# Kernel tuning notes

Hardware: AMD Instinct MI355X
Metric: run time of the kernel (lower is better)

The kernel has to match this reference:

```python
import jax, jax.numpy as jnp
import numpy as np

N_DIM = 512
HIDDEN = 512


def setup_inputs() -> dict:
    key = jax.random.key(0)
    ks = jax.random.split(key, 9)
    s = 0.02
    x = jax.random.normal(ks[0], (4, 4096, N_DIM), dtype=jnp.float32)
    Wq = jax.random.normal(ks[1], (N_DIM, HIDDEN), dtype=jnp.float32) * s
    bq = jnp.zeros((HIDDEN,), dtype=jnp.float32)
    Wk = jax.random.normal(ks[2], (N_DIM, HIDDEN), dtype=jnp.float32) * s
    bk = jnp.zeros((HIDDEN,), dtype=jnp.float32)
    Wv = jax.random.normal(ks[3], (N_DIM, HIDDEN), dtype=jnp.float32) * s
    bv = jnp.zeros((HIDDEN,), dtype=jnp.float32)
    Wo = jax.random.normal(ks[4], (HIDDEN, N_DIM), dtype=jnp.float32) * s
    bo = jnp.zeros((N_DIM,), dtype=jnp.float32)
    return {"x": x, "Wq": Wq, "bq": bq, "Wk": Wk, "bk": bk,
            "Wv": Wv, "bv": bv, "Wo": Wo, "bo": bo}


def reference(x, Wq, bq, Wk, bk, Wv, bv, Wo, bo):
    # x: [B, S, n_dim]
    q = jnp.einsum('bsd,dh->bsh', x, Wq) + bq  # [B,S,H]
    k = jnp.einsum('bsd,dh->bsh', x, Wk) + bk
    v = jnp.einsum('bsd,dh->bsh', x, Wv) + bv
    # NOTE: original module uses UNSCALED scores (no 1/sqrt(d))
    scores = jnp.einsum('bqh,bkh->bqk', q, k)  # [B,S,S]
    attn = jax.nn.softmax(scores, axis=-1)
    y = jnp.einsum('bqk,bkh->bqh', attn, v)
    return jnp.einsum('bsh,hd->bsd', y, Wo) + bo
```

## Files before the change

kernel.cpp:

```cpp
#include <hip/hip_runtime.h>
#include <hip/hip_bf16.h>

typedef _Float16 h8 __attribute__((ext_vector_type(8)));
typedef __bf16   b8 __attribute__((ext_vector_type(8)));
typedef float    f4 __attribute__((ext_vector_type(4)));

#define B_    4
#define S_    4096
#define D_    512
#define ROWS_ (B_ * S_)
#define NQKV_ 1536
#define BR    64
#define BC    32
#define KP    520
#define PP    40
#define NIT   (S_ / BC)
#define KTILE (BC * KP)
#define MSH   (30.0f * 1.4426950408889634f)
#define L2E   1.4426950408889634f

__device__ __forceinline__ void gl_lds16(const void* src, void* dst) {
    __builtin_amdgcn_global_load_lds(
        (const __attribute__((address_space(1))) unsigned int*)src,
        (__attribute__((address_space(3))) unsigned int*)dst, 16, 0, 0);
}

__global__ __launch_bounds__(256) void convert_all(
    const float* __restrict__ x,
    const float* __restrict__ Wq, const float* __restrict__ Wk, const float* __restrict__ Wv,
    const float* __restrict__ bq, const float* __restrict__ bk, const float* __restrict__ bv,
    const float* __restrict__ Wo,
    _Float16* __restrict__ xh, _Float16* __restrict__ wqkvT, _Float16* __restrict__ woT,
    float* __restrict__ bqkv)
{
    long i0 = (long)blockIdx.x * blockDim.x + threadIdx.x;
    long stride = (long)gridDim.x * blockDim.x;
    const long NX  = (long)ROWS_ * D_;
    const long NW  = (long)D_ * NQKV_;
    const long NWO = (long)D_ * D_;

    for (long i = i0; i < NX; i += stride) xh[i] = (_Float16)x[i];

    for (long i = i0; i < NW; i += stride) {
        long n = i >> 9, k = i & 511;
        long which = n >> 9, nn = n & 511;
        const float* W = (which == 0) ? Wq : (which == 1) ? Wk : Wv;
        wqkvT[i] = (_Float16)W[k * 512 + nn];
    }
    for (long i = i0; i < NWO; i += stride) {
        long n = i >> 9, k = i & 511;
        woT[i] = (_Float16)Wo[k * 512 + n];
    }
    for (long i = i0; i < NQKV_; i += stride) {
        long which = i >> 9, nn = i & 511;
        const float* bb = (which == 0) ? bq : (which == 1) ? bk : bv;
        bqkv[i] = bb[nn];
    }
}

#define GP 40
template <bool OUT_F16>
__global__ __launch_bounds__(256) void gemm_bt(
    const _Float16* __restrict__ A, const _Float16* __restrict__ BT,
    const float* __restrict__ bias, void* __restrict__ Cout,
    int M, int N, int K)
{
    __shared__ _Float16 As[128 * GP];
    __shared__ _Float16 Bs[128 * GP];

    int tid = threadIdx.x;
    int w = tid >> 6, lane = tid & 63, quad = lane >> 4, l16 = lane & 15;
    long row0 = (long)blockIdx.x * 128, col0 = (long)blockIdx.y * 128;
    int wr = (w >> 1) * 64, wc = (w & 1) * 64;

    f4 acc[4][4];
    for (int i = 0; i < 4; i++)
        for (int j = 0; j < 4; j++) acc[i][j] = (f4){0.f, 0.f, 0.f, 0.f};

    int sr = tid >> 1, sc = (tid & 1) * 16;
    for (int k0 = 0; k0 < K; k0 += 32) {
        __syncthreads();
        {
            const h8* ga = (const h8*)(A  + (row0 + sr) * K + k0 + sc);
            const h8* gb = (const h8*)(BT + (col0 + sr) * K + k0 + sc);
            *(h8*)(As + sr * GP + sc)     = ga[0];
            *(h8*)(As + sr * GP + sc + 8) = ga[1];
            *(h8*)(Bs + sr * GP + sc)     = gb[0];
            *(h8*)(Bs + sr * GP + sc + 8) = gb[1];
        }
        __syncthreads();
        h8 af[4], bf[4];
        for (int i = 0; i < 4; i++) af[i] = *(const h8*)(As + (wr + i * 16 + l16) * GP + quad * 8);
        for (int j = 0; j < 4; j++) bf[j] = *(const h8*)(Bs + (wc + j * 16 + l16) * GP + quad * 8);
        for (int i = 0; i < 4; i++)
            for (int j = 0; j < 4; j++)
                acc[i][j] = __builtin_amdgcn_mfma_f32_16x16x32_f16(af[i], bf[j], acc[i][j], 0, 0, 0);
    }
    for (int i = 0; i < 4; i++)
        for (int j = 0; j < 4; j++)
            for (int r = 0; r < 4; r++) {
                long row = row0 + wr + i * 16 + quad * 4 + r;
                long col = col0 + wc + j * 16 + l16;
                float v = acc[i][j][r] + bias[col];
                if (OUT_F16) ((_Float16*)Cout)[row * N + col] = (_Float16)v;
                else         ((float*)Cout)[row * N + col]    = v;
            }
}

__global__ __launch_bounds__(256) void pack_v(const _Float16* __restrict__ qkv,
                                              __bf16* __restrict__ vP)
{
    __shared__ _Float16 T[32 * 520];
    int kt = blockIdx.x, b = blockIdx.y;
    int t = threadIdx.x;

    const _Float16* src = qkv + ((long)b * S_ + kt * 32 + (t >> 3)) * NQKV_ + 1024;
#pragma unroll
    for (int i = 0; i < 8; i++) {
        int c = (t & 7) + i * 8;
        *(h8*)(T + (t >> 3) * 520 + c * 8) = *(const h8*)(src + c * 8);
    }
    __syncthreads();

    __bf16* dst = vP + (((long)b * 128 + kt) * 32) * 512;
#pragma unroll
    for (int i = 0; i < 8; i++) {
        int c = t + i * 256;
        int dt = c >> 6, q = (c >> 4) & 3, l = c & 15;
        b8 out;
#pragma unroll
        for (int k3 = 0; k3 < 8; k3++)
            out[k3] = (__bf16)(float)T[(q * 8 + k3) * 520 + dt * 16 + l];
        *(b8*)(dst + (long)c * 8) = out;
    }
}

__global__ __launch_bounds__(512, 2) void attn_kernel(const _Float16* __restrict__ qkv,
                                                      const __bf16* __restrict__ vP,
                                                      _Float16* __restrict__ yb)
{
    __shared__ _Float16 Ks[4 * KTILE];
    __shared__ __bf16   Ps[2 * BR * PP];
    __shared__ float    lpart[2][BR];

    const int tid = threadIdx.x;
    const int w = tid >> 6, lane = tid & 63, quad = lane >> 4, l16 = lane & 15;

    const int bid = blockIdx.x;
    const int xcd = bid & 7;
    const int b = xcd >> 1;
    const long q0 = (long)((xcd & 1) * 32 + (bid >> 3)) * BR;
    const long rowBase = (long)b * S_;

    const _Float16* kbase = qkv + rowBase * NQKV_ + 512;

    if (w < 4) {
        const int rs0 = (w & 1) * 32;
        const int kh  = w >> 1;

        h8 Qf0[16], Qf1[16];
        {
            const _Float16* q0p = qkv + (rowBase + q0 + rs0 + l16) * NQKV_;
            const _Float16* q1p = qkv + (rowBase + q0 + rs0 + 16 + l16) * NQKV_;
#pragma unroll
            for (int ks = 0; ks < 16; ks++) {
                Qf0[ks] = *(const h8*)(q0p + ks * 32 + quad * 8);
                Qf1[ks] = *(const h8*)(q1p + ks * 32 + quad * 8);
            }
        }
#pragma unroll
        for (int t = 0; t < 2; t++)
#pragma unroll
            for (int i = 0; i < 4; i++) {
                int r = w * 4 + i;
                gl_lds16(kbase + (long)(t * BC + r) * NQKV_ + lane * 8,
                         Ks + t * KTILE + r * KP);
            }
        float lo0[4] = {0.f, 0.f, 0.f, 0.f};
        float lo1[4] = {0.f, 0.f, 0.f, 0.f};

        __syncthreads();

        for (int kt = 0; kt < NIT; kt++) {
            if (kt + 2 < NIT) {
                const _Float16* kn = kbase + (long)(kt + 2) * BC * NQKV_;
                _Float16* kd = Ks + ((kt + 2) & 3) * KTILE;
#pragma unroll
                for (int i = 0; i < 4; i++) {
                    int r = w * 4 + i;
                    gl_lds16(kn + (long)r * NQKV_ + lane * 8, kd + r * KP);
                }
            }
            f4 Sa0 = (f4){0.f, 0.f, 0.f, 0.f}, Sa1 = (f4){0.f, 0.f, 0.f, 0.f};
            f4 Sb0 = (f4){0.f, 0.f, 0.f, 0.f}, Sb1 = (f4){0.f, 0.f, 0.f, 0.f};
            const _Float16* krow = Ks + (kt & 3) * KTILE + (kh * 16 + l16) * KP + quad * 8;
            __builtin_amdgcn_s_setprio(1);
#pragma unroll
            for (int ks = 0; ks < 8; ks++) {
                h8 kb0 = *(const h8*)(krow + ks * 32);
                h8 kb1 = *(const h8*)(krow + (ks + 8) * 32);
                Sa0 = __builtin_amdgcn_mfma_f32_16x16x32_f16(Qf0[ks],     kb0, Sa0, 0, 0, 0);
                Sb0 = __builtin_amdgcn_mfma_f32_16x16x32_f16(Qf1[ks],     kb0, Sb0, 0, 0, 0);
                Sa1 = __builtin_amdgcn_mfma_f32_16x16x32_f16(Qf0[ks + 8], kb1, Sa1, 0, 0, 0);
                Sb1 = __builtin_amdgcn_mfma_f32_16x16x32_f16(Qf1[ks + 8], kb1, Sb1, 0, 0, 0);
            }
            __builtin_amdgcn_s_setprio(0);
            __bf16* ps = Ps + (kt & 1) * (BR * PP);
#pragma unroll
            for (int r = 0; r < 4; r++) {
                float p0 = exp2f((Sa0[r] + Sa1[r]) * L2E - MSH);
                float p1 = exp2f((Sb0[r] + Sb1[r]) * L2E - MSH);
                __bf16 pb0 = (__bf16)p0, pb1 = (__bf16)p1;
                ps[(rs0 + quad * 4 + r) * PP + kh * 16 + l16] = pb0;
                ps[(rs0 + 16 + quad * 4 + r) * PP + kh * 16 + l16] = pb1;
                lo0[r] += (float)pb0;
                lo1[r] += (float)pb1;
            }
            __builtin_amdgcn_sched_barrier(0);
            if (kt < NIT - 2) asm volatile("s_waitcnt vmcnt(4)");
            else              asm volatile("s_waitcnt vmcnt(0)");
            asm volatile("s_waitcnt lgkmcnt(0)");
            __builtin_amdgcn_s_barrier();
            __builtin_amdgcn_sched_barrier(0);
        }

#pragma unroll
        for (int r = 0; r < 4; r++)
#pragma unroll
            for (int m = 1; m < 16; m <<= 1) {
                lo0[r] += __shfl_xor(lo0[r], m, 16);
                lo1[r] += __shfl_xor(lo1[r], m, 16);
            }
        if (l16 == 0)
            for (int r = 0; r < 4; r++) {
                lpart[kh][rs0 + quad * 4 + r]      = lo0[r];
                lpart[kh][rs0 + 16 + quad * 4 + r] = lo1[r];
            }
        __syncthreads();
    } else {
        const int cv = w - 4;
        const __bf16* vpbase = vP + ((long)b * 128 * 32 + cv * 8) * 512 + lane * 8;

#pragma unroll
        for (int t = 0; t < 2; t++)
#pragma unroll
            for (int i = 0; i < 4; i++) {
                int r = w * 4 + i;
                gl_lds16(kbase + (long)(t * BC + r) * NQKV_ + lane * 8,
                         Ks + t * KTILE + r * KP);
            }
        b8 vA[8], vB[8];
#pragma unroll
        for (int ct = 0; ct < 8; ct++)
            vA[ct] = *(const b8*)(vpbase + ct * 512);

        f4 O[4][8];
#pragma unroll
        for (int rt = 0; rt < 4; rt++)
#pragma unroll
            for (int ct = 0; ct < 8; ct++) O[rt][ct] = (f4){0.f, 0.f, 0.f, 0.f};

        __syncthreads();

#define CONS_BODY(KT, VUSE, VLOAD)                                              \
  {                                                                             \
    const int kt_ = (KT);                                                       \
    if (kt_ + 1 < NIT) {                                                        \
      const __bf16* vs = vpbase + (long)(kt_ + 1) * (32 * 512);                 \
      _Pragma("unroll")                                                         \
      for (int ct = 0; ct < 8; ct++)                                            \
        VLOAD[ct] = *(const b8*)(vs + ct * 512);                                \
    }                                                                           \
    if (kt_ + 2 < NIT) {                                                        \
      const _Float16* kn = kbase + (long)(kt_ + 2) * BC * NQKV_;                \
      _Float16* kd = Ks + ((kt_ + 2) & 3) * KTILE;                              \
      _Pragma("unroll")                                                         \
      for (int i = 0; i < 4; i++) {                                             \
        int r = w * 4 + i;                                                      \
        gl_lds16(kn + (long)r * NQKV_ + lane * 8, kd + r * KP);                 \
      }                                                                         \
    }                                                                           \
    __builtin_amdgcn_sched_barrier(0);                                          \
    if (kt_ < NIT - 2)       asm volatile("s_waitcnt vmcnt(12)");               \
    else if (kt_ == NIT - 2) asm volatile("s_waitcnt vmcnt(8)");                \
    else                     asm volatile("s_waitcnt vmcnt(0)");                \
    asm volatile("s_waitcnt lgkmcnt(0)");                                       \
    __builtin_amdgcn_s_barrier();                                               \
    __builtin_amdgcn_sched_barrier(0);                                          \
    const __bf16* ps = Ps + (kt_ & 1) * (BR * PP);                              \
    b8 pa[4];                                                                   \
    _Pragma("unroll")                                                           \
    for (int rt = 0; rt < 4; rt++)                                              \
      pa[rt] = *(const b8*)(ps + (rt * 16 + l16) * PP + quad * 8);              \
    __builtin_amdgcn_s_setprio(1);                                              \
    _Pragma("unroll")                                                           \
    for (int ct = 0; ct < 8; ct++)                                              \
      _Pragma("unroll")                                                         \
      for (int rt = 0; rt < 4; rt++)                                            \
        O[rt][ct] = __builtin_amdgcn_mfma_f32_16x16x32_bf16(pa[rt], VUSE[ct], O[rt][ct], 0, 0, 0); \
    __builtin_amdgcn_s_setprio(0);                                              \
  }

        for (int kt = 0; kt < NIT; kt += 2) {
            CONS_BODY(kt,     vA, vB);
            CONS_BODY(kt + 1, vB, vA);
        }
#undef CONS_BODY

        __syncthreads();

#pragma unroll
        for (int rt = 0; rt < 4; rt++) {
            f4 l0 = *(const f4*)(&lpart[0][rt * 16 + quad * 4]);
            f4 l1 = *(const f4*)(&lpart[1][rt * 16 + quad * 4]);
            float li[4];
            for (int r = 0; r < 4; r++) li[r] = 1.f / (l0[r] + l1[r]);
            for (int ct = 0; ct < 8; ct++)
                for (int r = 0; r < 4; r++) {
                    long row = rowBase + q0 + rt * 16 + quad * 4 + r;
                    long col = cv * 128 + ct * 16 + l16;
                    yb[row * 512 + col] = (_Float16)(O[rt][ct][r] * li[r]);
                }
        }
    }
}

extern "C" void kernel_launch(void* const* d_in, const int* in_sizes, int n_in,
                              void* d_out, int out_size, void* d_ws, size_t ws_size,
                              hipStream_t stream)
{
    const float* x  = (const float*)d_in[0];
    const float* Wq = (const float*)d_in[1];
    const float* bq = (const float*)d_in[2];
    const float* Wk = (const float*)d_in[3];
    const float* bk = (const float*)d_in[4];
    const float* Wv = (const float*)d_in[5];
    const float* bv = (const float*)d_in[6];
    const float* Wo = (const float*)d_in[7];
    const float* bo = (const float*)d_in[8];
    float* out = (float*)d_out;

    char* ws = (char*)d_ws;
    _Float16* xh    = (_Float16*)(ws);
    _Float16* qkv   = (_Float16*)(ws + 16777216);
    __bf16*   vP    = (__bf16*)(ws + 67108864);
    _Float16* yb    = (_Float16*)(ws + 83886080);
    _Float16* wqkvT = (_Float16*)(ws + 100663296);
    _Float16* woT   = (_Float16*)(ws + 102236160);
    float*    bqkv  = (float*)(ws + 102760448);

    convert_all<<<2048, 256, 0, stream>>>(x, Wq, Wk, Wv, bq, bk, bv, Wo,
                                          xh, wqkvT, woT, bqkv);

    dim3 g1(128, 12);
    gemm_bt<true><<<g1, 256, 0, stream>>>(xh, wqkvT, bqkv, qkv, ROWS_, NQKV_, D_);

    dim3 gp(128, 4);
    pack_v<<<gp, 256, 0, stream>>>(qkv, vP);

    attn_kernel<<<256, 512, 0, stream>>>(qkv, vP, yb);

    dim3 g2(128, 4);
    gemm_bt<false><<<g2, 256, 0, stream>>>(yb, woT, bo, out, ROWS_, D_, D_);
}
```

Measured before the change: 320.9 us.

## Fuse V packing into QKV GEMM epilogue and widen attention key tile to 64

The QKV GEMM epilogue now writes the V columns directly in the packed bf16 layout the attention kernel reads, so the separate pack_v kernel and its extra pass over V go away. The attention kernel moves from 32-key to 64-key tiles with a double-buffered K tile and a 514-element padded row stride. The consumer warps are restructured to issue the P·V MFMAs for the previous tile while loading V for the current one. This halves the number of barrier iterations, at the cost of more LDS, more registers, and a shallower K prefetch depth (two buffers instead of four) with a full vmcnt(0) wait each iteration.

```diff
diff --git a/kernel.cpp b/kernel.cpp
--- a/kernel.cpp
+++ b/kernel.cpp
@@ -11,11 +11,11 @@
 #define ROWS_ (B_ * S_)
 #define NQKV_ 1536
 #define BR    64
-#define BC    32
-#define KP    520
-#define PP    40
-#define NIT   (S_ / BC)
-#define KTILE (BC * KP)
+#define BC2   64
+#define NIT2  (S_ / BC2)
+#define KP2   514
+#define KT2   (BC2 * KP2)
+#define PP2   66
 #define MSH   (30.0f * 1.4426950408889634f)
 #define L2E   1.4426950408889634f
 
@@ -63,7 +63,7 @@
 __global__ __launch_bounds__(256) void gemm_bt(
     const _Float16* __restrict__ A, const _Float16* __restrict__ BT,
     const float* __restrict__ bias, void* __restrict__ Cout,
-    int M, int N, int K)
+    int M, int N, int K, __bf16* __restrict__ vPout)
 {
     __shared__ _Float16 As[128 * GP];
     __shared__ _Float16 Bs[128 * GP];
@@ -96,42 +96,36 @@
             for (int j = 0; j < 4; j++)
                 acc[i][j] = __builtin_amdgcn_mfma_f32_16x16x32_f16(af[i], bf[j], acc[i][j], 0, 0, 0);
     }
-    for (int i = 0; i < 4; i++)
-        for (int j = 0; j < 4; j++)
-            for (int r = 0; r < 4; r++) {
-                long row = row0 + wr + i * 16 + quad * 4 + r;
-                long col = col0 + wc + j * 16 + l16;
-                float v = acc[i][j][r] + bias[col];
-                if (OUT_F16) ((_Float16*)Cout)[row * N + col] = (_Float16)v;
-                else         ((float*)Cout)[row * N + col]    = v;
-            }
-}
-
-__global__ __launch_bounds__(256) void pack_v(const _Float16* __restrict__ qkv,
-                                              __bf16* __restrict__ vP)
-{
-    __shared__ _Float16 T[32 * 520];
-    int kt = blockIdx.x, b = blockIdx.y;
-    int t = threadIdx.x;
-
-    const _Float16* src = qkv + ((long)b * S_ + kt * 32 + (t >> 3)) * NQKV_ + 1024;
-#pragma unroll
-    for (int i = 0; i < 8; i++) {
-        int c = (t & 7) + i * 8;
-        *(h8*)(T + (t >> 3) * 520 + c * 8) = *(const h8*)(src + c * 8);
-    }
-    __syncthreads();
-
-    __bf16* dst = vP + (((long)b * 128 + kt) * 32) * 512;
-#pragma unroll
-    for (int i = 0; i < 8; i++) {
-        int c = t + i * 256;
-        int dt = c >> 6, q = (c >> 4) & 3, l = c & 15;
-        b8 out;
-#pragma unroll
-        for (int k3 = 0; k3 < 8; k3++)
-            out[k3] = (__bf16)(float)T[(q * 8 + k3) * 520 + dt * 16 + l];
-        *(b8*)(dst + (long)c * 8) = out;
+
+    if (OUT_F16 && vPout != nullptr && col0 >= 1024) {
+        for (int i = 0; i < 4; i++) {
+            long row = row0 + wr + i * 16 + quad * 4;
+            int bb   = (int)(row >> 12);
+            int s    = (int)(row & 4095);
+            int kt32 = s >> 5;
+            int qq   = (s >> 3) & 3;
+            int k3   = s & 7;
+            for (int j = 0; j < 4; j++) {
+                int dglob = (int)(col0 - 1024) + wc + j * 16;
+                int dt = dglob >> 4;
+                long off = (((long)bb * 128 + kt32) * 32 + dt) * 512
+                         + (qq * 16 + l16) * 8 + k3;
+                union { __bf16 h[4]; uint2 u2; } pk;
+                for (int r = 0; r < 4; r++)
+                    pk.h[r] = (__bf16)(acc[i][j][r] + bias[col0 + wc + j * 16 + l16]);
+                *(uint2*)(vPout + off) = pk.u2;
+            }
+        }
+    } else {
+        for (int i = 0; i < 4; i++)
+            for (int j = 0; j < 4; j++)
+                for (int r = 0; r < 4; r++) {
+                    long row = row0 + wr + i * 16 + quad * 4 + r;
+                    long col = col0 + wc + j * 16 + l16;
+                    float v = acc[i][j][r] + bias[col];
+                    if (OUT_F16) ((_Float16*)Cout)[row * N + col] = (_Float16)v;
+                    else         ((float*)Cout)[row * N + col]    = v;
+                }
     }
 }
 
@@ -139,8 +133,8 @@
                                                       const __bf16* __restrict__ vP,
                                                       _Float16* __restrict__ yb)
 {
-    __shared__ _Float16 Ks[4 * KTILE];
-    __shared__ __bf16   Ps[2 * BR * PP];
+    __shared__ _Float16 Ks[2 * KT2];
+    __shared__ __bf16   Ps[2 * BR * PP2];
     __shared__ float    lpart[2][BR];
 
     const int tid = threadIdx.x;
@@ -154,71 +148,87 @@
 
     const _Float16* kbase = qkv + rowBase * NQKV_ + 512;
 
+#pragma unroll
+    for (int i = 0; i < 8; i++) {
+        int r = w * 8 + i;
+        gl_lds16(kbase + (long)r * NQKV_ + lane * 8, Ks + r * KP2);
+    }
+
     if (w < 4) {
         const int rs0 = (w & 1) * 32;
-        const int kh  = w >> 1;
+        const int kg0 = (w >> 1) * 32;
 
         h8 Qf0[16], Qf1[16];
         {
             const _Float16* q0p = qkv + (rowBase + q0 + rs0 + l16) * NQKV_;
-            const _Float16* q1p = qkv + (rowBase + q0 + rs0 + 16 + l16) * NQKV_;
+            const _Float16* q1p = q0p + 16 * NQKV_;
 #pragma unroll
             for (int ks = 0; ks < 16; ks++) {
                 Qf0[ks] = *(const h8*)(q0p + ks * 32 + quad * 8);
                 Qf1[ks] = *(const h8*)(q1p + ks * 32 + quad * 8);
             }
         }
-#pragma unroll
-        for (int t = 0; t < 2; t++)
-#pragma unroll
-            for (int i = 0; i < 4; i++) {
-                int r = w * 4 + i;
-                gl_lds16(kbase + (long)(t * BC + r) * NQKV_ + lane * 8,
-                         Ks + t * KTILE + r * KP);
-            }
         float lo0[4] = {0.f, 0.f, 0.f, 0.f};
         float lo1[4] = {0.f, 0.f, 0.f, 0.f};
 
         __syncthreads();
 
-        for (int kt = 0; kt < NIT; kt++) {
-            if (kt + 2 < NIT) {
-                const _Float16* kn = kbase + (long)(kt + 2) * BC * NQKV_;
-                _Float16* kd = Ks + ((kt + 2) & 3) * KTILE;
-#pragma unroll
-                for (int i = 0; i < 4; i++) {
-                    int r = w * 4 + i;
-                    gl_lds16(kn + (long)r * NQKV_ + lane * 8, kd + r * KP);
-                }
-            }
-            f4 Sa0 = (f4){0.f, 0.f, 0.f, 0.f}, Sa1 = (f4){0.f, 0.f, 0.f, 0.f};
-            f4 Sb0 = (f4){0.f, 0.f, 0.f, 0.f}, Sb1 = (f4){0.f, 0.f, 0.f, 0.f};
-            const _Float16* krow = Ks + (kt & 3) * KTILE + (kh * 16 + l16) * KP + quad * 8;
+        for (int kt = 0; kt < NIT2; kt++) {
+            if (kt + 1 < NIT2) {
+                const _Float16* kn = kbase + (long)(kt + 1) * BC2 * NQKV_;
+                _Float16* kd = Ks + ((kt + 1) & 1) * KT2;
+#pragma unroll
+                for (int i = 0; i < 8; i++) {
+                    int r = w * 8 + i;
+                    gl_lds16(kn + (long)r * NQKV_ + lane * 8, kd + r * KP2);
+                }
+            }
+            f4 S[2][2][2];
+#pragma unroll
+            for (int a = 0; a < 2; a++)
+#pragma unroll
+                for (int c = 0; c < 2; c++)
+#pragma unroll
+                    for (int d = 0; d < 2; d++) S[a][c][d] = (f4){0.f, 0.f, 0.f, 0.f};
+            const _Float16* kr0 = Ks + (kt & 1) * KT2 + (kg0 + l16) * KP2 + quad * 8;
+            const _Float16* kr1 = kr0 + 16 * KP2;
             __builtin_amdgcn_s_setprio(1);
 #pragma unroll
             for (int ks = 0; ks < 8; ks++) {
-                h8 kb0 = *(const h8*)(krow + ks * 32);
-                h8 kb1 = *(const h8*)(krow + (ks + 8) * 32);
-                Sa0 = __builtin_amdgcn_mfma_f32_16x16x32_f16(Qf0[ks],     kb0, Sa0, 0, 0, 0);
-                Sb0 = __builtin_amdgcn_mfma_f32_16x16x32_f16(Qf1[ks],     kb0, Sb0, 0, 0, 0);
-                Sa1 = __builtin_amdgcn_mfma_f32_16x16x32_f16(Qf0[ks + 8], kb1, Sa1, 0, 0, 0);
-                Sb1 = __builtin_amdgcn_mfma_f32_16x16x32_f16(Qf1[ks + 8], kb1, Sb1, 0, 0, 0);
+                h8 a0 = *(const h8*)(kr0 + ks * 32);
+                h8 a1 = *(const h8*)(kr0 + (ks + 8) * 32);
+                h8 c0 = *(const h8*)(kr1 + ks * 32);
+                h8 c1 = *(const h8*)(kr1 + (ks + 8) * 32);
+                S[0][0][0] = __builtin_amdgcn_mfma_f32_16x16x32_f16(Qf0[ks],     a0, S[0][0][0], 0, 0, 0);
+                S[1][0][0] = __builtin_amdgcn_mfma_f32_16x16x32_f16(Qf1[ks],     a0, S[1][0][0], 0, 0, 0);
+                S[0][1][0] = __builtin_amdgcn_mfma_f32_16x16x32_f16(Qf0[ks],     c0, S[0][1][0], 0, 0, 0);
+                S[1][1][0] = __builtin_amdgcn_mfma_f32_16x16x32_f16(Qf1[ks],     c0, S[1][1][0], 0, 0, 0);
+                S[0][0][1] = __builtin_amdgcn_mfma_f32_16x16x32_f16(Qf0[ks + 8], a1, S[0][0][1], 0, 0, 0);
+                S[1][0][1] = __builtin_amdgcn_mfma_f32_16x16x32_f16(Qf1[ks + 8], a1, S[1][0][1], 0, 0, 0);
+                S[0][1][1] = __builtin_amdgcn_mfma_f32_16x16x32_f16(Qf0[ks + 8], c1, S[0][1][1], 0, 0, 0);
+                S[1][1][1] = __builtin_amdgcn_mfma_f32_16x16x32_f16(Qf1[ks + 8], c1, S[1][1][1], 0, 0, 0);
             }
             __builtin_amdgcn_s_setprio(0);
-            __bf16* ps = Ps + (kt & 1) * (BR * PP);
+            __bf16* ps = Ps + (kt & 1) * (BR * PP2);
 #pragma unroll
             for (int r = 0; r < 4; r++) {
-                float p0 = exp2f((Sa0[r] + Sa1[r]) * L2E - MSH);
-                float p1 = exp2f((Sb0[r] + Sb1[r]) * L2E - MSH);
-                __bf16 pb0 = (__bf16)p0, pb1 = (__bf16)p1;
-                ps[(rs0 + quad * 4 + r) * PP + kh * 16 + l16] = pb0;
-                ps[(rs0 + 16 + quad * 4 + r) * PP + kh * 16 + l16] = pb1;
-                lo0[r] += (float)pb0;
-                lo1[r] += (float)pb1;
+                float p00 = exp2f((S[0][0][0][r] + S[0][0][1][r]) * L2E - MSH);
+                float p01 = exp2f((S[0][1][0][r] + S[0][1][1][r]) * L2E - MSH);
+                float p10 = exp2f((S[1][0][0][r] + S[1][0][1][r]) * L2E - MSH);
+                float p11 = exp2f((S[1][1][0][r] + S[1][1][1][r]) * L2E - MSH);
+                __bf16 b00 = (__bf16)p00, b01 = (__bf16)p01;
+                __bf16 b10 = (__bf16)p10, b11 = (__bf16)p11;
+                int r0 = (rs0 + quad * 4 + r) * PP2;
+                int r1 = (rs0 + 16 + quad * 4 + r) * PP2;
+                ps[r0 + kg0 + l16]      = b00;
+                ps[r0 + kg0 + 16 + l16] = b01;
+                ps[r1 + kg0 + l16]      = b10;
+                ps[r1 + kg0 + 16 + l16] = b11;
+                lo0[r] += (float)b00 + (float)b01;
+                lo1[r] += (float)b10 + (float)b11;
             }
             __builtin_amdgcn_sched_barrier(0);
-            if (kt < NIT - 2) asm volatile("s_waitcnt vmcnt(4)");
-            else              asm volatile("s_waitcnt vmcnt(0)");
+            asm volatile("s_waitcnt vmcnt(0)");
             asm volatile("s_waitcnt lgkmcnt(0)");
             __builtin_amdgcn_s_barrier();
             __builtin_amdgcn_sched_barrier(0);
@@ -233,80 +243,77 @@
             }
         if (l16 == 0)
             for (int r = 0; r < 4; r++) {
-                lpart[kh][rs0 + quad * 4 + r]      = lo0[r];
-                lpart[kh][rs0 + 16 + quad * 4 + r] = lo1[r];
+                lpart[w >> 1][rs0 + quad * 4 + r]      = lo0[r];
+                lpart[w >> 1][rs0 + 16 + quad * 4 + r] = lo1[r];
             }
         __syncthreads();
     } else {
         const int cv = w - 4;
         const __bf16* vpbase = vP + ((long)b * 128 * 32 + cv * 8) * 512 + lane * 8;
 
-#pragma unroll
-        for (int t = 0; t < 2; t++)
-#pragma unroll
-            for (int i = 0; i < 4; i++) {
-                int r = w * 4 + i;
-                gl_lds16(kbase + (long)(t * BC + r) * NQKV_ + lane * 8,
-                         Ks + t * KTILE + r * KP);
-            }
-        b8 vA[8], vB[8];
-#pragma unroll
-        for (int ct = 0; ct < 8; ct++)
-            vA[ct] = *(const b8*)(vpbase + ct * 512);
-
         f4 O[4][8];
 #pragma unroll
         for (int rt = 0; rt < 4; rt++)
 #pragma unroll
             for (int ct = 0; ct < 8; ct++) O[rt][ct] = (f4){0.f, 0.f, 0.f, 0.f};
-
-        __syncthreads();
-
-#define CONS_BODY(KT, VUSE, VLOAD)                                              \
-  {                                                                             \
-    const int kt_ = (KT);                                                       \
-    if (kt_ + 1 < NIT) {                                                        \
-      const __bf16* vs = vpbase + (long)(kt_ + 1) * (32 * 512);                 \
-      _Pragma("unroll")                                                         \
-      for (int ct = 0; ct < 8; ct++)                                            \
-        VLOAD[ct] = *(const b8*)(vs + ct * 512);                                \
-    }                                                                           \
-    if (kt_ + 2 < NIT) {                                                        \
-      const _Float16* kn = kbase + (long)(kt_ + 2) * BC * NQKV_;                \
-      _Float16* kd = Ks + ((kt_ + 2) & 3) * KTILE;                              \
-      _Pragma("unroll")                                                         \
-      for (int i = 0; i < 4; i++) {                                             \
-        int r = w * 4 + i;                                                      \
-        gl_lds16(kn + (long)r * NQKV_ + lane * 8, kd + r * KP);                 \
-      }                                                                         \
-    }                                                                           \
-    __builtin_amdgcn_sched_barrier(0);                                          \
-    if (kt_ < NIT - 2)       asm volatile("s_waitcnt vmcnt(12)");               \
-    else if (kt_ == NIT - 2) asm volatile("s_waitcnt vmcnt(8)");                \
-    else                     asm volatile("s_waitcnt vmcnt(0)");                \
-    asm volatile("s_waitcnt lgkmcnt(0)");                                       \
-    __builtin_amdgcn_s_barrier();                                               \
-    __builtin_amdgcn_sched_barrier(0);                                          \
-    const __bf16* ps = Ps + (kt_ & 1) * (BR * PP);                              \
-    b8 pa[4];                                                                   \
-    _Pragma("unroll")                                                           \
-    for (int rt = 0; rt < 4; rt++)                                              \
-      pa[rt] = *(const b8*)(ps + (rt * 16 + l16) * PP + quad * 8);              \
-    __builtin_amdgcn_s_setprio(1);                                              \
-    _Pragma("unroll")                                                           \
-    for (int ct = 0; ct < 8; ct++)                                              \
-      _Pragma("unroll")                                                         \
-      for (int rt = 0; rt < 4; rt++)                                            \
-        O[rt][ct] = __builtin_amdgcn_mfma_f32_16x16x32_bf16(pa[rt], VUSE[ct], O[rt][ct], 0, 0, 0); \
-    __builtin_amdgcn_s_setprio(0);                                              \
-  }
-
-        for (int kt = 0; kt < NIT; kt += 2) {
-            CONS_BODY(kt,     vA, vB);
-            CONS_BODY(kt + 1, vB, vA);
-        }
-#undef CONS_BODY
-
+        b8 vreg[16];
+
+        __syncthreads();
+
+        for (int kt = 0; kt < NIT2; kt++) {
+            asm volatile("s_waitcnt vmcnt(0)");
+            if (kt + 1 < NIT2) {
+                const _Float16* kn = kbase + (long)(kt + 1) * BC2 * NQKV_;
+                _Float16* kd = Ks + ((kt + 1) & 1) * KT2;
+#pragma unroll
+                for (int i = 0; i < 8; i++) {
+                    int r = w * 8 + i;
+                    gl_lds16(kn + (long)r * NQKV_ + lane * 8, kd + r * KP2);
+                }
+            }
+            if (kt > 0) {
+                const __bf16* ps = Ps + ((kt - 1) & 1) * (BR * PP2);
+                __builtin_amdgcn_s_setprio(1);
+#pragma unroll
+                for (int rt = 0; rt < 4; rt++) {
+                    b8 pa0 = *(const b8*)(ps + (rt * 16 + l16) * PP2 + quad * 8);
+                    b8 pa1 = *(const b8*)(ps + (rt * 16 + l16) * PP2 + 32 + quad * 8);
+#pragma unroll
+                    for (int ct = 0; ct < 8; ct++) {
+                        O[rt][ct] = __builtin_amdgcn_mfma_f32_16x16x32_bf16(pa0, vreg[ct],     O[rt][ct], 0, 0, 0);
+                        O[rt][ct] = __builtin_amdgcn_mfma_f32_16x16x32_bf16(pa1, vreg[8 + ct], O[rt][ct], 0, 0, 0);
+                    }
+                }
+                __builtin_amdgcn_s_setprio(0);
+            }
+            {
+                const __bf16* vs0 = vpbase + (long)(2 * kt) * (32 * 512);
+#pragma unroll
+                for (int ct = 0; ct < 8; ct++) {
+                    vreg[ct]     = *(const b8*)(vs0 + ct * 512);
+                    vreg[8 + ct] = *(const b8*)(vs0 + 32 * 512 + ct * 512);
+                }
+            }
+            __builtin_amdgcn_sched_barrier(0);
+            asm volatile("s_waitcnt vmcnt(16)");
+            asm volatile("s_waitcnt lgkmcnt(0)");
+            __builtin_amdgcn_s_barrier();
+            __builtin_amdgcn_sched_barrier(0);
+        }
+        asm volatile("s_waitcnt vmcnt(0)");
+        {
+            const __bf16* ps = Ps + ((NIT2 - 1) & 1) * (BR * PP2);
+#pragma unroll
+            for (int rt = 0; rt < 4; rt++) {
+                b8 pa0 = *(const b8*)(ps + (rt * 16 + l16) * PP2 + quad * 8);
+                b8 pa1 = *(const b8*)(ps + (rt * 16 + l16) * PP2 + 32 + quad * 8);
+#pragma unroll
+                for (int ct = 0; ct < 8; ct++) {
+                    O[rt][ct] = __builtin_amdgcn_mfma_f32_16x16x32_bf16(pa0, vreg[ct],     O[rt][ct], 0, 0, 0);
+                    O[rt][ct] = __builtin_amdgcn_mfma_f32_16x16x32_bf16(pa1, vreg[8 + ct], O[rt][ct], 0, 0, 0);
+                }
+            }
+        }
         __syncthreads();
 
 #pragma unroll
@@ -353,13 +360,10 @@
                                           xh, wqkvT, woT, bqkv);
 
     dim3 g1(128, 12);
-    gemm_bt<true><<<g1, 256, 0, stream>>>(xh, wqkvT, bqkv, qkv, ROWS_, NQKV_, D_);
-
-    dim3 gp(128, 4);
-    pack_v<<<gp, 256, 0, stream>>>(qkv, vP);
+    gemm_bt<true><<<g1, 256, 0, stream>>>(xh, wqkvT, bqkv, qkv, ROWS_, NQKV_, D_, vP);
 
     attn_kernel<<<256, 512, 0, stream>>>(qkv, vP, yb);
 
     dim3 g2(128, 4);
-    gemm_bt<false><<<g2, 256, 0, stream>>>(yb, woT, bo, out, ROWS_, D_, D_);
-}
+    gemm_bt<false><<<g2, 256, 0, stream>>>(yb, woT, bo, out, ROWS_, D_, D_, nullptr);
+}
```

After: 517.8 us. 61.4% more time.
